# Kernel optimization log

Measured on AMD Instinct MI355X. Metric: run time of the kernel, lower is better.

Reference implementation:

```python
import jax, jax.numpy as jnp
import numpy as np

D_MODEL = 1024
N_HEADS = 16


def setup_inputs() -> dict:
    key = jax.random.key(0)
    k1, k2, k3 = jax.random.split(key, 3)
    x = jax.random.normal(k1, (4, 2048, D_MODEL), dtype=jnp.float32)
    # torch nn.Linear(D, 3D): weight (3D, D), bias (3D)
    W = jax.random.normal(k2, (3 * D_MODEL, D_MODEL), dtype=jnp.float32) * (D_MODEL ** -0.5)
    b = jax.random.normal(k3, (3 * D_MODEL,), dtype=jnp.float32) * 0.01
    return {"x": x, "W": W, "b": b}


def reference(x, W, b):
    N, C, D = x.shape
    H = N_HEADS
    hd = D // H
    z = jnp.einsum("ncd,ed->nce", x, W) + b  # [N, C, 3D]
    k = z[:, :, :D].reshape(N, C, H, hd).transpose(0, 2, 1, 3)
    q = z[:, :, D:2 * D].reshape(N, C, H, hd).transpose(0, 2, 1, 3)
    v = z[:, :, 2 * D:].reshape(N, C, H, hd).transpose(0, 2, 1, 3)
    # NOTE: original scales by full model dim D, not head dim
    scores = jnp.einsum("nhqd,nhkd->nhqk", q, k) * (D ** -0.5)
    causal = jnp.tril(jnp.ones((C, C), dtype=bool))
    scores = jnp.where(causal[None, None], scores, -jnp.inf)
    attn = jax.nn.softmax(scores, axis=-1)
    out = jnp.einsum("nhqk,nhkd->nhqd", attn, v)
    return out.transpose(0, 2, 1, 3).reshape(N, C, D)
```

## Files before the change

kernel.cpp:

```cpp
#include <hip/hip_runtime.h>
#include <hip/hip_bf16.h>

typedef __bf16 bf16;
typedef __bf16 bf16x8 __attribute__((ext_vector_type(8)));
typedef float f32x4 __attribute__((ext_vector_type(4)));
typedef unsigned int u32x4 __attribute__((ext_vector_type(4)));

#define SEQ   2048
#define NBAT  4
#define DM    1024
#define NH    16
#define HD    64
#define E3    3072

__global__ void cvt2_bf16_kernel(const float* __restrict__ a, bf16* __restrict__ oa, int na8,
                                 const float* __restrict__ b, bf16* __restrict__ ob, int nb8) {
  const int stride = gridDim.x * blockDim.x;
  const int ntot = na8 + nb8;
  for (int i = blockIdx.x * blockDim.x + threadIdx.x; i < ntot; i += stride) {
    const float* src;
    bf16* dst;
    int j;
    if (i < na8) { src = a; dst = oa; j = i; }
    else         { src = b; dst = ob; j = i - na8; }
    const float4* p = (const float4*)(src + (size_t)j * 8);
    float4 x = p[0];
    float4 y = p[1];
    bf16x8 o;
    o[0] = (bf16)x.x; o[1] = (bf16)x.y; o[2] = (bf16)x.z; o[3] = (bf16)x.w;
    o[4] = (bf16)y.x; o[5] = (bf16)y.y; o[6] = (bf16)y.z; o[7] = (bf16)y.w;
    *(bf16x8*)(dst + (size_t)j * 8) = o;
  }
}

#define BM 128
#define BN 128
#define BK 32
#define KSTEPS (DM / BK)

__global__ __launch_bounds__(256, 2) void qkv_gemm_kernel(
    const bf16* __restrict__ A, const bf16* __restrict__ B,
    const float* __restrict__ bias, bf16* __restrict__ Z)
{
  __shared__ bf16 sA[2][BM * BK];
  __shared__ bf16 sB[2][BN * BK];

  const int tid  = threadIdx.x;
  const int lane = tid & 63;
  const int w    = tid >> 6;
  const int wr   = w >> 1;
  const int wc   = w & 1;
  const int m0   = blockIdx.x * BM;
  const int n0   = blockIdx.y * BN;

  const f32x4 z4 = {0.f, 0.f, 0.f, 0.f};
  f32x4 acc[4][4];
#pragma unroll
  for (int i = 0; i < 4; ++i)
#pragma unroll
    for (int j = 0; j < 4; ++j)
      acc[i][j] = z4;

  const int srow = w * 32 + (lane >> 2);
  const int skk  = (lane & 3) * 8;
  const bf16* gA = A + (size_t)m0 * DM;
  const bf16* gB = B + (size_t)n0 * DM;

  auto stage = [&](int buf, int t) {
    const int k0 = t * BK;
#pragma unroll
    for (int c = 0; c < 2; ++c)
      __builtin_amdgcn_global_load_lds(
          (const __attribute__((address_space(1))) unsigned int*)(gA + (size_t)(srow + c * 16) * DM + k0 + skk),
          (__attribute__((address_space(3))) unsigned int*)(&sA[buf][w * 1024 + c * 512]),
          16, 0, 0);
#pragma unroll
    for (int c = 0; c < 2; ++c)
      __builtin_amdgcn_global_load_lds(
          (const __attribute__((address_space(1))) unsigned int*)(gB + (size_t)(srow + c * 16) * DM + k0 + skk),
          (__attribute__((address_space(3))) unsigned int*)(&sB[buf][w * 1024 + c * 512]),
          16, 0, 0);
  };

  stage(0, 0);
  int cur = 0;
  const int arow = wr * 64 + (lane & 15);
  const int brow = wc * 64 + (lane & 15);
  const int kf   = (lane >> 4) * 8;

  for (int t = 0; t < KSTEPS; ++t) {
    __syncthreads();
    if (t + 1 < KSTEPS) stage(cur ^ 1, t + 1);
    bf16x8 af[4], bfr[4];
#pragma unroll
    for (int i = 0; i < 4; ++i)
      af[i] = *(const bf16x8*)&sA[cur][(arow + i * 16) * BK + kf];
#pragma unroll
    for (int j = 0; j < 4; ++j)
      bfr[j] = *(const bf16x8*)&sB[cur][(brow + j * 16) * BK + kf];
#pragma unroll
    for (int i = 0; i < 4; ++i)
#pragma unroll
      for (int j = 0; j < 4; ++j)
        acc[i][j] = __builtin_amdgcn_mfma_f32_16x16x32_bf16(af[i], bfr[j], acc[i][j], 0, 0, 0);
    cur ^= 1;
  }

#pragma unroll
  for (int i = 0; i < 4; ++i) {
#pragma unroll
    for (int j = 0; j < 4; ++j) {
      const int col = n0 + wc * 64 + j * 16 + (lane & 15);
      const float bb = bias[col];
#pragma unroll
      for (int r = 0; r < 4; ++r) {
        const int row = m0 + wr * 64 + i * 16 + (lane >> 4) * 4 + r;
        Z[(size_t)row * E3 + col] = (bf16)(acc[i][j][r] + bb);
      }
    }
  }
}

#define QB 128
#define KB 64
#define NQT (SEQ / QB)

__global__ __launch_bounds__(256, 2) void attn_kernel(
    const bf16* __restrict__ Z, float* __restrict__ out)
{
  __shared__ bf16 sK[2][KB][64];
  __shared__ bf16 sVT[2][HD][64];

  const int tid   = threadIdx.x;
  const int lane  = tid & 63;
  const int w     = tid >> 6;
  const int l15   = lane & 15;
  const int lhi   = lane >> 4;
  const int l7    = l15 & 7;
  const int e2    = l15 >> 3;

  const int flat  = blockIdx.x;
  const int xcd   = flat & 7;
  const int idx   = flat >> 3;
  const int ctx   = xcd * 8 + (idx & 7);
  const int pairb = idx >> 3;
  const int h     = ctx & 15;
  const int n     = ctx >> 4;

  const size_t zb = (size_t)n * SEQ * E3;
  const int kcol0 = h * HD;
  const int qcol0 = DM + h * HD;
  const int vcol0 = 2 * DM + h * HD;

  const f32x4 z4 = {0.f, 0.f, 0.f, 0.f};
  const f32x4 neg4 = {-1e32f, -1e32f, -1e32f, -1e32f};
  const float scale = 0.03125f;
  const float L2E   = 1.4426950408889634f;
  const float SL2E  = scale * L2E;

  const u32x4 onesu = {0x3F803F80u, 0x3F803F80u, 0x3F803F80u, 0x3F803F80u};
  const bf16x8 onesf = __builtin_bit_cast(bf16x8, onesu);

  const int c0row = tid >> 3;
  const int t7    = tid & 7;
  const int c0col = t7 * 8;
  const int sgk = ((c0row & 12) << 1) | ((c0row & 16) >> 2) | (c0row & 3);

  const int krow_in = lane >> 3;
  const int kdblk   = ((lane & 7) ^ (lane >> 3)) * 8;

  const size_t ob = (size_t)n * SEQ * DM;

  bf16x8 vpre[2];
  auto vload = [&](int t) {
#pragma unroll
    for (int c = 0; c < 2; ++c)
      vpre[c] = *(const bf16x8*)&Z[zb + (size_t)(t * KB + c0row + 32 * c) * E3 + vcol0 + c0col];
  };
  auto lwriteV = [&](int buf) {
#pragma unroll
    for (int c = 0; c < 2; ++c)
#pragma unroll
      for (int j = 0; j < 8; ++j)
        sVT[buf][c0col + j][(sgk + 32 * c) ^ ((j ^ t7) << 3)] = vpre[c][j];
  };
  auto stageK = [&](int t, int buf) {
#pragma unroll
    for (int c = 0; c < 2; ++c) {
      const int cc = 2 * w + c;
      __builtin_amdgcn_global_load_lds(
          (const __attribute__((address_space(1))) unsigned int*)(
              Z + zb + (size_t)(t * KB + 8 * cc + krow_in) * E3 + kcol0 + kdblk),
          (__attribute__((address_space(3))) unsigned int*)(&sK[buf][8 * cc][0]),
          16, 0, 0);
    }
  };

#pragma unroll 1
  for (int phase = 0; phase < 2; ++phase) {
    const int qtile = phase == 0 ? pairb : (NQT - 1 - pairb);
    const int qwave = qtile * QB + w * 32;
    const int T     = 2 * qtile + 2;

    bf16x8 qf[2][2];
#pragma unroll
    for (int qs = 0; qs < 2; ++qs) {
      const int qrow = qwave + qs * 16 + l15;
#pragma unroll
      for (int kk = 0; kk < 2; ++kk)
        qf[qs][kk] = *(const bf16x8*)&Z[zb + (size_t)qrow * E3 + qcol0 + kk * 32 + lhi * 8];
    }

    f32x4 accO[2][4];
    f32x4 accL[2];
#pragma unroll
    for (int qs = 0; qs < 2; ++qs) {
#pragma unroll
      for (int dt = 0; dt < 4; ++dt) accO[qs][dt] = z4;
      accL[qs] = z4;
    }

    stageK(0, 0);
    vload(0);
    lwriteV(0);
    vload(1);
    __syncthreads();

#pragma unroll 1
    for (int t = 0; t < T; ++t) {
      const int cur = t & 1;
      if (t + 1 < T) { stageK(t + 1, cur ^ 1); lwriteV(cur ^ 1); }
      if (t + 2 < T) vload(t + 2);

      f32x4 st[2][4];
      __builtin_amdgcn_s_setprio(1);
#pragma unroll
      for (int kt = 0; kt < 4; ++kt) {
        const int blk0 = (lhi ^ l7) * 8;
        const int blk1 = ((4 + lhi) ^ l7) * 8;
        bf16x8 kf0 = *(const bf16x8*)&sK[cur][kt * 16 + l15][blk0];
        bf16x8 kf1 = *(const bf16x8*)&sK[cur][kt * 16 + l15][blk1];
#pragma unroll
        for (int qs = 0; qs < 2; ++qs) {
          st[qs][kt] = __builtin_amdgcn_mfma_f32_16x16x32_bf16(kf0, qf[qs][0], z4, 0, 0, 0);
          st[qs][kt] = __builtin_amdgcn_mfma_f32_16x16x32_bf16(kf1, qf[qs][1], st[qs][kt], 0, 0, 0);
        }
      }
      __builtin_amdgcn_s_setprio(0);

      if (t >= 2 * qtile) {
        const int tb = 4 * (t - 2 * qtile);
#pragma unroll
        for (int qs = 0; qs < 2; ++qs) {
          const int dgq = 2 * w + qs;
#pragma unroll
          for (int kt = 0; kt < 4; ++kt) {
            const int fg = tb + kt;
            if (fg > dgq) st[qs][kt] = neg4;
            else if (fg == dgq) {
#pragma unroll
              for (int r = 0; r < 4; ++r)
                if (lhi * 4 + r > l15) st[qs][kt][r] = -1e32f;
            }
          }
        }
      }

      bf16x8 pb[2][2];
#pragma unroll
      for (int qs = 0; qs < 2; ++qs)
#pragma unroll
        for (int c = 0; c < 2; ++c) {
          u32x4 pu;
#pragma unroll
          for (int i = 0; i < 4; ++i) {
            const int kt = 2 * c + (i >> 1);
            const int r  = (2 * i) & 3;
            const float p0 = exp2f(st[qs][kt][r]     * SL2E);
            const float p1 = exp2f(st[qs][kt][r + 1] * SL2E);
            const bf16 b0v = (bf16)p0;
            const bf16 b1v = (bf16)p1;
            pu[i] = (unsigned int)__builtin_bit_cast(unsigned short, b0v)
                  | ((unsigned int)__builtin_bit_cast(unsigned short, b1v) << 16);
          }
          pb[qs][c] = __builtin_bit_cast(bf16x8, pu);
        }

      __builtin_amdgcn_s_setprio(1);
#pragma unroll
      for (int c = 0; c < 2; ++c)
#pragma unroll
        for (int qs = 0; qs < 2; ++qs)
          accL[qs] = __builtin_amdgcn_mfma_f32_16x16x32_bf16(onesf, pb[qs][c], accL[qs], 0, 0, 0);

#pragma unroll
      for (int c = 0; c < 2; ++c) {
#pragma unroll
        for (int dt = 0; dt < 4; ++dt) {
          const int idxv = ((4 * c + lhi) ^ (l7 ^ ((2 * dt + e2) & 7))) << 3;
          const bf16x8 av = *(const bf16x8*)&sVT[cur][dt * 16 + l15][idxv];
#pragma unroll
          for (int qs = 0; qs < 2; ++qs)
            accO[qs][dt] = __builtin_amdgcn_mfma_f32_16x16x32_bf16(av, pb[qs][c], accO[qs][dt], 0, 0, 0);
        }
      }
      __builtin_amdgcn_s_setprio(0);

      __syncthreads();
    }

#pragma unroll
    for (int qs = 0; qs < 2; ++qs) {
      const float inv  = 1.f / accL[qs][0];
      const int   qrow = qwave + qs * 16 + l15;
#pragma unroll
      for (int dt = 0; dt < 4; ++dt) {
        float4 o;
        o.x = accO[qs][dt][0] * inv;
        o.y = accO[qs][dt][1] * inv;
        o.z = accO[qs][dt][2] * inv;
        o.w = accO[qs][dt][3] * inv;
        *(float4*)&out[ob + (size_t)qrow * DM + h * HD + dt * 16 + lhi * 4] = o;
      }
    }
  }
}

extern "C" void kernel_launch(void* const* d_in, const int* in_sizes, int n_in,
                              void* d_out, int out_size, void* d_ws, size_t ws_size,
                              hipStream_t stream) {
  const float* x    = (const float*)d_in[0];
  const float* W    = (const float*)d_in[1];
  const float* bias = (const float*)d_in[2];
  float* out = (float*)d_out;

  bf16* xb = (bf16*)d_ws;
  bf16* Wb = xb + (size_t)NBAT * SEQ * DM;
  bf16* Zb = Wb + (size_t)E3 * DM;

  cvt2_bf16_kernel<<<1536, 256, 0, stream>>>(x, xb, NBAT * SEQ * DM / 8,
                                             W, Wb, E3 * DM / 8);

  dim3 g1(NBAT * SEQ / BM, E3 / BN);
  qkv_gemm_kernel<<<g1, 256, 0, stream>>>(xb, Wb, bias, Zb);

  attn_kernel<<<512, 256, 0, stream>>>(Zb, out);
}
```

Measured before the change: 158.9 us.

## Write V transposed and pre-swizzled from GEMM epilogue, stage via direct LDS loads

The QKV GEMM epilogue now writes K/Q into a narrower 2048-wide buffer and writes V directly in a per-head transposed, key-permuted layout. The attention kernel then stages V into LDS with async global_load_lds like K, replacing the register-staged load plus scalar transpose scatter into shared memory. This removes per-element LDS writes and register pressure in the attention loop. The cost is a scattered 8-byte store pattern in the GEMM epilogue for V, and correctness depends on the permutation matching the old LDS layout.

```diff
diff --git a/kernel.cpp b/kernel.cpp
--- a/kernel.cpp
+++ b/kernel.cpp
@@ -2,6 +2,7 @@
 #include <hip/hip_bf16.h>
 
 typedef __bf16 bf16;
+typedef __bf16 bf16x4 __attribute__((ext_vector_type(4)));
 typedef __bf16 bf16x8 __attribute__((ext_vector_type(8)));
 typedef float f32x4 __attribute__((ext_vector_type(4)));
 typedef unsigned int u32x4 __attribute__((ext_vector_type(4)));
@@ -12,6 +13,7 @@
 #define NH    16
 #define HD    64
 #define E3    3072
+#define E2    2048
 
 __global__ void cvt2_bf16_kernel(const float* __restrict__ a, bf16* __restrict__ oa, int na8,
                                  const float* __restrict__ b, bf16* __restrict__ ob, int nb8) {
@@ -40,7 +42,7 @@
 
 __global__ __launch_bounds__(256, 2) void qkv_gemm_kernel(
     const bf16* __restrict__ A, const bf16* __restrict__ B,
-    const float* __restrict__ bias, bf16* __restrict__ Z)
+    const float* __restrict__ bias, bf16* __restrict__ Z2, bf16* __restrict__ VT)
 {
   __shared__ bf16 sA[2][BM * BK];
   __shared__ bf16 sB[2][BN * BK];
@@ -106,16 +108,38 @@
     cur ^= 1;
   }
 
-#pragma unroll
-  for (int i = 0; i < 4; ++i) {
-#pragma unroll
-    for (int j = 0; j < 4; ++j) {
-      const int col = n0 + wc * 64 + j * 16 + (lane & 15);
-      const float bb = bias[col];
-#pragma unroll
-      for (int r = 0; r < 4; ++r) {
-        const int row = m0 + wr * 64 + i * 16 + (lane >> 4) * 4 + r;
-        Z[(size_t)row * E3 + col] = (bf16)(acc[i][j][r] + bb);
+  if (n0 < 2048) {
+#pragma unroll
+    for (int i = 0; i < 4; ++i) {
+#pragma unroll
+      for (int j = 0; j < 4; ++j) {
+        const int col = n0 + wc * 64 + j * 16 + (lane & 15);
+        const float bb = bias[col];
+#pragma unroll
+        for (int r = 0; r < 4; ++r) {
+          const int row = m0 + wr * 64 + i * 16 + (lane >> 4) * 4 + r;
+          Z2[(size_t)row * E2 + col] = (bf16)(acc[i][j][r] + bb);
+        }
+      }
+    }
+  } else {
+#pragma unroll
+    for (int i = 0; i < 4; ++i) {
+      const int rowb = m0 + wr * 64 + i * 16 + (lane >> 4) * 4;
+      const int nb   = rowb >> 11;
+      const int k    = rowb & 2047;
+      const int ksig = (k & ~63) | (k & 32) | (((k >> 2) & 3) << 3) | (((k >> 4) & 1) << 2);
+#pragma unroll
+      for (int j = 0; j < 4; ++j) {
+        const int col  = n0 + wc * 64 + j * 16 + (lane & 15);
+        const float bb = bias[col];
+        const int colv = col - 2048;
+        const int h    = colv >> 6;
+        const int d    = colv & 63;
+        bf16x4 v4;
+#pragma unroll
+        for (int r = 0; r < 4; ++r) v4[r] = (bf16)(acc[i][j][r] + bb);
+        *(bf16x4*)&VT[(((size_t)nb * NH + h) * HD + d) * SEQ + ksig] = v4;
       }
     }
   }
@@ -126,7 +150,7 @@
 #define NQT (SEQ / QB)
 
 __global__ __launch_bounds__(256, 2) void attn_kernel(
-    const bf16* __restrict__ Z, float* __restrict__ out)
+    const bf16* __restrict__ Z2, const bf16* __restrict__ VT, float* __restrict__ out)
 {
   __shared__ bf16 sK[2][KB][64];
   __shared__ bf16 sVT[2][HD][64];
@@ -147,10 +171,10 @@
   const int h     = ctx & 15;
   const int n     = ctx >> 4;
 
-  const size_t zb = (size_t)n * SEQ * E3;
+  const size_t zb2 = (size_t)n * SEQ * E2;
+  const size_t vtb = ((size_t)n * NH + h) * HD * SEQ;
   const int kcol0 = h * HD;
   const int qcol0 = DM + h * HD;
-  const int vcol0 = 2 * DM + h * HD;
 
   const f32x4 z4 = {0.f, 0.f, 0.f, 0.f};
   const f32x4 neg4 = {-1e32f, -1e32f, -1e32f, -1e32f};
@@ -161,37 +185,32 @@
   const u32x4 onesu = {0x3F803F80u, 0x3F803F80u, 0x3F803F80u, 0x3F803F80u};
   const bf16x8 onesf = __builtin_bit_cast(bf16x8, onesu);
 
-  const int c0row = tid >> 3;
-  const int t7    = tid & 7;
-  const int c0col = t7 * 8;
-  const int sgk = ((c0row & 12) << 1) | ((c0row & 16) >> 2) | (c0row & 3);
-
   const int krow_in = lane >> 3;
   const int kdblk   = ((lane & 7) ^ (lane >> 3)) * 8;
 
   const size_t ob = (size_t)n * SEQ * DM;
 
-  bf16x8 vpre[2];
-  auto vload = [&](int t) {
-#pragma unroll
-    for (int c = 0; c < 2; ++c)
-      vpre[c] = *(const bf16x8*)&Z[zb + (size_t)(t * KB + c0row + 32 * c) * E3 + vcol0 + c0col];
-  };
-  auto lwriteV = [&](int buf) {
-#pragma unroll
-    for (int c = 0; c < 2; ++c)
-#pragma unroll
-      for (int j = 0; j < 8; ++j)
-        sVT[buf][c0col + j][(sgk + 32 * c) ^ ((j ^ t7) << 3)] = vpre[c][j];
-  };
   auto stageK = [&](int t, int buf) {
 #pragma unroll
     for (int c = 0; c < 2; ++c) {
       const int cc = 2 * w + c;
       __builtin_amdgcn_global_load_lds(
           (const __attribute__((address_space(1))) unsigned int*)(
-              Z + zb + (size_t)(t * KB + 8 * cc + krow_in) * E3 + kcol0 + kdblk),
+              Z2 + zb2 + (size_t)(t * KB + 8 * cc + krow_in) * E2 + kcol0 + kdblk),
           (__attribute__((address_space(3))) unsigned int*)(&sK[buf][8 * cc][0]),
+          16, 0, 0);
+    }
+  };
+  auto stageV = [&](int t, int buf) {
+#pragma unroll
+    for (int c = 0; c < 2; ++c) {
+      const int cc   = 2 * w + c;
+      const int dsrc = 8 * cc + (lane >> 3);
+      const int blk  = (lane & 7) ^ ((dsrc ^ (dsrc >> 3)) & 7);
+      __builtin_amdgcn_global_load_lds(
+          (const __attribute__((address_space(1))) unsigned int*)(
+              VT + vtb + (size_t)dsrc * SEQ + t * KB + blk * 8),
+          (__attribute__((address_space(3))) unsigned int*)(&sVT[buf][8 * cc][0]),
           16, 0, 0);
     }
   };
@@ -208,7 +227,7 @@
       const int qrow = qwave + qs * 16 + l15;
 #pragma unroll
       for (int kk = 0; kk < 2; ++kk)
-        qf[qs][kk] = *(const bf16x8*)&Z[zb + (size_t)qrow * E3 + qcol0 + kk * 32 + lhi * 8];
+        qf[qs][kk] = *(const bf16x8*)&Z2[zb2 + (size_t)qrow * E2 + qcol0 + kk * 32 + lhi * 8];
     }
 
     f32x4 accO[2][4];
@@ -221,16 +240,13 @@
     }
 
     stageK(0, 0);
-    vload(0);
-    lwriteV(0);
-    vload(1);
+    stageV(0, 0);
     __syncthreads();
 
 #pragma unroll 1
     for (int t = 0; t < T; ++t) {
       const int cur = t & 1;
-      if (t + 1 < T) { stageK(t + 1, cur ^ 1); lwriteV(cur ^ 1); }
-      if (t + 2 < T) vload(t + 2);
+      if (t + 1 < T) { stageK(t + 1, cur ^ 1); stageV(t + 1, cur ^ 1); }
 
       f32x4 st[2][4];
       __builtin_amdgcn_s_setprio(1);
@@ -336,13 +352,14 @@
 
   bf16* xb = (bf16*)d_ws;
   bf16* Wb = xb + (size_t)NBAT * SEQ * DM;
-  bf16* Zb = Wb + (size_t)E3 * DM;
+  bf16* Z2 = Wb + (size_t)E3 * DM;
+  bf16* VT = Z2 + (size_t)NBAT * SEQ * E2;
 
   cvt2_bf16_kernel<<<1536, 256, 0, stream>>>(x, xb, NBAT * SEQ * DM / 8,
                                              W, Wb, E3 * DM / 8);
 
   dim3 g1(NBAT * SEQ / BM, E3 / BN);
-  qkv_gemm_kernel<<<g1, 256, 0, stream>>>(xb, Wb, bias, Zb);
-
-  attn_kernel<<<512, 256, 0, stream>>>(Zb, out);
+  qkv_gemm_kernel<<<g1, 256, 0, stream>>>(xb, Wb, bias, Z2, VT);
+
+  attn_kernel<<<512, 256, 0, stream>>>(Z2, VT, out);
 }
```

Result: faster. 154.9 us (-2.5%).
